# Optimization experiments

Measured on AMD Instinct MI355X. Metric: run time of the kernel, lower is better.

Reference implementation:

```python
import jax, jax.numpy as jnp
import numpy as np

N = 8192
IN_DIM = 512
MEM_DIM = 512


def _linear_params(k, fan_in, fan_out):
    kw, kb = jax.random.split(k)
    s = 1.0 / np.sqrt(fan_in)
    W = jax.random.uniform(kw, (fan_in, fan_out), jnp.float32, -s, s)
    b = jax.random.uniform(kb, (fan_out,), jnp.float32, -s, s)
    return W, b


def setup_inputs() -> dict:
    key = jax.random.key(0)
    ks = jax.random.split(key, 12)
    inputs = jax.random.normal(ks[0], (N, IN_DIM), jnp.float32)
    # tree.type is a [1,2] mixing matrix per node (lang vs vis weights)
    type_mask = jax.nn.softmax(jax.random.normal(ks[1], (N, 2), jnp.float32), axis=-1)
    # topologically ordered tree: parent slot of node i is in [0, i]; slot 0 = virtual zero root state
    rng = np.random.default_rng(0)
    parent = np.zeros(N, dtype=np.int32)
    for i in range(1, N):
        parent[i] = rng.integers(0, i + 1)
    d = {"inputs": inputs, "type_mask": type_mask, "parent": jnp.asarray(parent)}
    names = ["ioux_vis", "iouh_vis", "fx_vis", "fh_vis",
             "ioux_lang", "iouh_lang", "fx_lang", "fh_lang"]
    fanins = [IN_DIM, MEM_DIM, IN_DIM, MEM_DIM] * 2
    fanouts = [3 * MEM_DIM, 3 * MEM_DIM, MEM_DIM, MEM_DIM] * 2
    for j, nm in enumerate(names):
        W, b = _linear_params(ks[2 + j], fanins[j], fanouts[j])
        d["W_" + nm] = W
        d["b_" + nm] = b
    return d


def reference(inputs, type_mask, parent,
              W_ioux_vis, b_ioux_vis, W_iouh_vis, b_iouh_vis,
              W_fx_vis, b_fx_vis, W_fh_vis, b_fh_vis,
              W_ioux_lang, b_ioux_lang, W_iouh_lang, b_iouh_lang,
              W_fx_lang, b_fx_lang, W_fh_lang, b_fh_lang):
    n_nodes = inputs.shape[0]
    D = W_fh_vis.shape[1]
    # batch the input-dependent projections into big GEMMs (fused across all nodes)
    x_iou_v = inputs @ W_ioux_vis + b_ioux_vis  # [N, 3D]
    x_f_v = inputs @ W_fx_vis + b_fx_vis        # [N, D]
    x_iou_l = inputs @ W_ioux_lang + b_ioux_lang
    x_f_l = inputs @ W_fx_lang + b_fx_lang

    def node(x_iou, x_f, h_p, c_p, W_iouh, b_iouh, W_fh, b_fh):
        iou = x_iou + h_p @ W_iouh + b_iouh  # [3D]
        i, o, u = jnp.split(iou, 3)
        f = jax.nn.sigmoid(x_f + h_p @ W_fh + b_fh)
        c = jax.nn.sigmoid(i) * jnp.tanh(u) + f * c_p
        h = jax.nn.sigmoid(o) * jnp.tanh(c)
        return c, h

    # slot 0 holds the zero state used by root nodes; node i lives at slot i+1
    c0 = jnp.zeros((n_nodes + 1, D), inputs.dtype)
    h0 = jnp.zeros((n_nodes + 1, D), inputs.dtype)

    def step(carry, xs):
        c_all, h_all = carry
        n, p, xiv, xfv, xil, xfl, tm = xs
        h_p = h_all[p]
        c_p = c_all[p]
        c_v, h_v = node(xiv, xfv, h_p, c_p, W_iouh_vis, b_iouh_vis, W_fh_vis, b_fh_vis)
        c_l, h_l = node(xil, xfl, h_p, c_p, W_iouh_lang, b_iouh_lang, W_fh_lang, b_fh_lang)
        # type_mask @ cat([lang, vis]) == tm[0]*lang + tm[1]*vis
        c_n = tm[0] * c_l + tm[1] * c_v
        h_n = tm[0] * h_l + tm[1] * h_v  # dropout is identity in eval
        return (c_all.at[n + 1].set(c_n), h_all.at[n + 1].set(h_n)), None

    idx = jnp.arange(n_nodes)
    (c_all, h_all), _ = jax.lax.scan(
        step, (c0, h0), (idx, parent, x_iou_v, x_f_v, x_iou_l, x_f_l, type_mask))
    return c_all[1:], h_all[1:]
```

## Files before the change

### kernel.cpp

```cpp
#include <hip/hip_runtime.h>
#include <math.h>

typedef unsigned short ushort_t;
typedef unsigned int uint_t;
typedef unsigned long long u64_t;
typedef __attribute__((ext_vector_type(8))) short short8;
typedef __attribute__((ext_vector_type(4))) float f32x4;

#define N_NODES 8192
#define DIM 512
#define KTOT 1024
#define NCOLS 4096
#define BM 128
#define BN 128
#define NTILE (NCOLS / BN)
#define KIT (KTOT / 32)
#define WIMG_USHORTS ((size_t)NTILE * KIT * 4096)
#define MAXLEV_LDS 128
#define CSTRIDE 32

__device__ __forceinline__ float sigm(float x) { return 1.0f / (1.0f + __expf(-x)); }
__device__ __forceinline__ float tanh_fast(float x) {
    float ax = fabsf(x);
    float e = __expf(2.0f * ax);
    float t = 1.0f - 2.0f / (e + 1.0f);
    return copysignf(t, x);
}
__device__ __forceinline__ uint_t packf(float f) {
    uint_t u = __float_as_uint(f);
    uint_t hi = u & 0xffff0000u;
    float r = f - __uint_as_float(hi);
    return hi | (__float_as_uint(r) >> 16);
}
__device__ __forceinline__ float unpackw(uint_t w) {
    return __uint_as_float(w & 0xffff0000u) + __uint_as_float(w << 16);
}
__device__ __forceinline__ uint_t rne16(float f) {
    uint_t u = __float_as_uint(f);
    return (u + 0x7fffu + ((u >> 16) & 1u)) >> 16;
}

__device__ __forceinline__ void fragAB_u32(const uint4 w0, const uint4 w1,
                                           short8& hi8, short8& lo8) {
    union { uint_t w[4]; short8 s; } H, L;
    uint_t u[8] = { w0.x, w0.y, w0.z, w0.w, w1.x, w1.y, w1.z, w1.w };
#pragma unroll
    for (int j = 0; j < 4; ++j) {
        H.w[j] = (u[2 * j + 1] & 0xffff0000u) | (u[2 * j] >> 16);
        L.w[j] = (u[2 * j + 1] << 16) | (u[2 * j] & 0xffffu);
    }
    hi8 = H.s; lo8 = L.s;
}

__device__ __forceinline__ void fragA_f32(const float4 f0, const float4 f1,
                                          short8& hi8, short8& lo8) {
    union { uint_t w[4]; short8 s; } H, L;
    float f[8] = { f0.x, f0.y, f0.z, f0.w, f1.x, f1.y, f1.z, f1.w };
#pragma unroll
    for (int j = 0; j < 4; ++j) {
        float a = f[2 * j], b = f[2 * j + 1];
        uint_t h0 = __float_as_uint(a) & 0xffff0000u;
        uint_t h1 = __float_as_uint(b) & 0xffff0000u;
        float r0 = a - __uint_as_float(h0);
        float r1 = b - __uint_as_float(h1);
        H.w[j] = h1 | (h0 >> 16);
        L.w[j] = (__float_as_uint(r1) & 0xffff0000u) | (__float_as_uint(r0) >> 16);
    }
    hi8 = H.s; lo8 = L.s;
}

__global__ void __launch_bounds__(256) prep_wimg_kernel(
    const float* __restrict__ Wx_iou_v, const float* __restrict__ Wh_iou_v,
    const float* __restrict__ Wx_f_v,   const float* __restrict__ Wh_f_v,
    const float* __restrict__ Wx_iou_l, const float* __restrict__ Wh_iou_l,
    const float* __restrict__ Wx_f_l,   const float* __restrict__ Wh_f_l,
    ushort_t* __restrict__ Wimg)
{
    __shared__ float T[32][132];
    int p = blockIdx.x >> 5, it = blockIdx.x & 31;
    int tid = threadIdx.x;
#pragma unroll
    for (int e = 0; e < 16; ++e) {
        int lin = e * 256 + tid;
        int dloc = lin & 15, kk = (lin >> 4) & 31, q = lin >> 9;
        int d = p * 16 + dloc;
        int qq = q & 3; bool lang = q >= 4;
        int k = it * 32 + kk;
        const float* W; int col, stride;
        if (qq < 3) { col = qq * DIM + d; stride = 3 * DIM;
            W = (k < DIM) ? (lang ? Wx_iou_l : Wx_iou_v) : (lang ? Wh_iou_l : Wh_iou_v); }
        else        { col = d; stride = DIM;
            W = (k < DIM) ? (lang ? Wx_f_l : Wx_f_v) : (lang ? Wh_f_l : Wh_f_v); }
        int kr = (k < DIM) ? k : (k - DIM);
        T[kk][dloc * 8 + q] = W[(size_t)kr * stride + col];
    }
    __syncthreads();
    size_t tilebase = (size_t)blockIdx.x * 4096;
#pragma unroll
    for (int gch = 0; gch < 2; ++gch) {
        int gi = gch * 256 + tid;
        int col = gi >> 2, gd = gi & 3;
        uint_t wds[4];
#pragma unroll
        for (int i = 0; i < 4; ++i) {
            uint_t v0 = rne16(T[gd * 8 + 2 * i][col]);
            uint_t v1 = rne16(T[gd * 8 + 2 * i + 1][col]);
            wds[i] = (v1 << 16) | v0;
        }
        *(uint4*)(Wimg + tilebase + (size_t)gi * 8) = make_uint4(wds[0], wds[1], wds[2], wds[3]);
    }
}

__global__ void prep_bias_kernel(
    const float* __restrict__ bx_iou_v, const float* __restrict__ bh_iou_v,
    const float* __restrict__ bx_f_v,   const float* __restrict__ bh_f_v,
    const float* __restrict__ bx_iou_l, const float* __restrict__ bh_iou_l,
    const float* __restrict__ bx_f_l,   const float* __restrict__ bh_f_l,
    float* __restrict__ bias)
{
    int j = blockIdx.x * blockDim.x + threadIdx.x;
    if (j >= NCOLS) return;
    int d = j >> 3, q = j & 7;
    int qq = q & 3;
    bool lang = (q & 4) != 0;
    const float* bx; const float* bh; int col;
    if (qq < 3) { col = qq * DIM + d; bx = lang ? bx_iou_l : bx_iou_v; bh = lang ? bh_iou_l : bh_iou_v; }
    else        { col = d;            bx = lang ? bx_f_l  : bx_f_v;   bh = lang ? bh_f_l  : bh_f_v; }
    bias[j] = bx[col] + bh[col];
}

__global__ void __launch_bounds__(1024) levels_sort_kernel(
    const int* __restrict__ parent,
    int* __restrict__ order, int* __restrict__ offsets,
    int* __restrict__ counts, int* __restrict__ cursors,
    int* __restrict__ nlev, int* __restrict__ tilestart,
    int* __restrict__ rbStart)
{
    __shared__ int s_level[N_NODES];
    __shared__ int s_assigned;
    __shared__ int s_maxlev;
    int tid = threadIdx.x;
    int pr[8];
#pragma unroll
    for (int ii = 0; ii < 8; ++ii) {
        int i = tid + ii * 1024;
        pr[ii] = parent[i];
        s_level[i] = -1;
    }
    for (int i = tid; i <= N_NODES; i += 1024) counts[i] = 0;
    if (tid == 0) { s_assigned = 0; s_maxlev = 0; }
    __syncthreads();

    for (int pass = 0; pass <= N_NODES; ++pass) {
        int newly = 0;
#pragma unroll
        for (int ii = 0; ii < 8; ++ii) {
            int i = tid + ii * 1024;
            if (s_level[i] < 0) {
                int p = pr[ii];
                if (p == 0) { s_level[i] = 0; newly++; }
                else { int lp = s_level[p - 1]; if (lp >= 0) { s_level[i] = lp + 1; newly++; } }
            }
        }
        if (newly) atomicAdd(&s_assigned, newly);
        __syncthreads();
        int a = s_assigned;
        if (a >= N_NODES) break;
        __syncthreads();
    }

#pragma unroll
    for (int ii = 0; ii < 8; ++ii) {
        int i = tid + ii * 1024;
        int lv = s_level[i];
        atomicAdd(&counts[lv], 1);
        atomicMax(&s_maxlev, lv);
    }
    __syncthreads();
    if (tid == 0) {
        int nl = s_maxlev + 1;
        nlev[0] = nl;
        int off = 0, toff = 0, rb = 0;
        for (int l = 0; l < nl; ++l) {
            offsets[l] = off; cursors[l] = off;
            tilestart[l] = toff; rbStart[l] = rb;
            int mt = (counts[l] + BM - 1) / BM;
            rb += mt;
            toff += mt * NTILE;
            off += counts[l];
        }
        offsets[nl] = off;
        tilestart[nl] = toff;
        rbStart[nl] = rb;
        nlev[1] = toff;
    }
    __syncthreads();
#pragma unroll
    for (int ii = 0; ii < 8; ++ii) {
        int i = tid + ii * 1024;
        int pos = atomicAdd(&cursors[s_level[i]], 1);
        order[pos] = i;
    }
}

__global__ void __launch_bounds__(512, 2) tree_fused_kernel(
    const float* __restrict__ inputs, const float* __restrict__ type_mask,
    const ushort_t* __restrict__ Wimg, const float* __restrict__ bias,
    const int* __restrict__ order, const int* __restrict__ offsets,
    const int* __restrict__ nlev, const int* __restrict__ parent,
    const int* __restrict__ rbStart,
    int* __restrict__ colCnt,
    uint_t* __restrict__ hPack, uint_t* __restrict__ cPack,
    float* __restrict__ out)
{
    float* cOut = out;
    float* hOut = out + (size_t)N_NODES * DIM;

    __shared__ float eps[BM * 132];
    __shared__ int s_node[BM];
    __shared__ int s_par[BM];
    __shared__ float s_tm[BM][2];
    __shared__ int s_rbs[MAXLEV_LDS];
    __shared__ int s_off[MAXLEV_LDS];

    int tid = threadIdx.x;
    int lane = tid & 63, w = tid >> 6;
    int wr = w >> 1, wc = w & 1;
    int l15 = lane & 15, g = lane >> 4;
    int nl = nlev[0];
    int total = nlev[1];

    int nload = nl + 1; if (nload > MAXLEV_LDS) nload = MAXLEV_LDS;
    for (int i = tid; i < nload; i += 512) { s_rbs[i] = rbStart[i]; s_off[i] = offsets[i]; }
    __syncthreads();

    const ushort_t* bLane = Wimg + (size_t)(wc * 64 + l15) * 32 + (size_t)g * 8;

#define LDB(RB, tilebase, itt) { \
    _Pragma("unroll") for (int n_ = 0; n_ < 4; ++n_) \
        RB[n_] = *(const uint4*)(bLane + (size_t)(tilebase + (itt)) * 4096 + n_ * 512); }

#define LDA_H(RA, itrel) { \
    _Pragma("unroll") for (int m_ = 0; m_ < 2; ++m_) { \
        const uint4* p_ = (const uint4*)(aBaseH[m_] + (itrel) * 32 + g * 8); \
        RA[m_][0] = p_[0]; RA[m_][1] = p_[1]; } }

#define LDA_X(RA, itt) { \
    _Pragma("unroll") for (int m_ = 0; m_ < 2; ++m_) { \
        const float4* p_ = (const float4*)(aBaseX[m_] + (itt) * 32 + g * 8); \
        RA[m_][0] = p_[0]; RA[m_][1] = p_[1]; } }

#define COMP_H(RA, RB) { \
    short8 bh_[4]; \
    _Pragma("unroll") for (int n_ = 0; n_ < 4; ++n_) { \
        union { uint4 u; short8 s; } c_; c_.u = RB[n_]; bh_[n_] = c_.s; } \
    _Pragma("unroll") for (int m_ = 0; m_ < 2; ++m_) { \
        short8 ah_, al_; fragAB_u32(RA[m_][0], RA[m_][1], ah_, al_); \
        _Pragma("unroll") for (int n_ = 0; n_ < 4; ++n_) { \
            acc[m_][n_] = __builtin_amdgcn_mfma_f32_16x16x32_bf16(ah_, bh_[n_], acc[m_][n_], 0, 0, 0); \
            acc[m_][n_] = __builtin_amdgcn_mfma_f32_16x16x32_bf16(al_, bh_[n_], acc[m_][n_], 0, 0, 0); } } }

#define COMP_X(RA, RB) { \
    short8 bh_[4]; \
    _Pragma("unroll") for (int n_ = 0; n_ < 4; ++n_) { \
        union { uint4 u; short8 s; } c_; c_.u = RB[n_]; bh_[n_] = c_.s; } \
    _Pragma("unroll") for (int m_ = 0; m_ < 2; ++m_) { \
        short8 ah_, al_; fragA_f32(RA[m_][0], RA[m_][1], ah_, al_); \
        _Pragma("unroll") for (int n_ = 0; n_ < 4; ++n_) { \
            acc[m_][n_] = __builtin_amdgcn_mfma_f32_16x16x32_bf16(ah_, bh_[n_], acc[m_][n_], 0, 0, 0); \
            acc[m_][n_] = __builtin_amdgcn_mfma_f32_16x16x32_bf16(al_, bh_[n_], acc[m_][n_], 0, 0, 0); } } }

#define POLL_ALL(colPrev, nPrev) { \
    int ok_ = 1; \
    if (lane < 32) { \
        int c_ = __hip_atomic_load(&(colPrev)[lane * CSTRIDE], __ATOMIC_RELAXED, \
                                   __HIP_MEMORY_SCOPE_AGENT); \
        ok_ = (c_ >= (nPrev)) ? 1 : 0; \
    } \
    uint_t cm_ = (uint_t)(__ballot(ok_) & 0xffffffffu); \
    uint_t gr_ = cm_ & (cm_ >> 1) & (cm_ >> 2) & (cm_ >> 3); \
    gmask = 0; \
    _Pragma("unroll") for (int g_ = 0; g_ < 8; ++g_) \
        gmask |= ((gr_ >> (4 * g_)) & 1u) << g_; }

#define WAVE_GATE(colPrev, nPrev, gq, slp) { \
    if (!(gmask & (1u << (gq)))) { \
        for (;;) { \
            POLL_ALL(colPrev, nPrev); \
            if (gmask & (1u << (gq))) break; \
            __builtin_amdgcn_s_sleep(slp); \
        } \
        asm volatile("" ::: "memory"); \
    } }

    for (int t = blockIdx.x; t < total; t += gridDim.x) {
        int lev = 0;
        while (lev + 1 < nload && s_rbs[lev + 1] * NTILE <= t) ++lev;
        int lt = t - s_rbs[lev] * NTILE;
        int ntile = lt % NTILE;
        int mt = lt / NTILE;
        int start = s_off[lev];
        int cnt = s_off[lev + 1] - start;
        int jc = ntile * BN;
        int r0 = mt * BM;
        int tbx = ntile * KIT;
        int tbh = ntile * KIT + 16;

        if (tid < BM) {
            int r = r0 + tid;
            int node = (r < cnt) ? order[start + r] : -1;
            s_node[tid] = node;
            int p = (node >= 0) ? parent[node] : 0;
            s_par[tid] = p;
            float t0 = 0.f, t1 = 0.f;
            if (node >= 0) { t0 = type_mask[node * 2]; t1 = type_mask[node * 2 + 1]; }
            s_tm[tid][0] = t0; s_tm[tid][1] = t1;
        }
        __syncthreads();

        f32x4 acc[2][4];
#pragma unroll
        for (int m = 0; m < 2; ++m)
#pragma unroll
            for (int n = 0; n < 4; ++n) acc[m][n] = (f32x4)(0.f);

        {
            const float* aBaseX[2];
#pragma unroll
            for (int m = 0; m < 2; ++m) {
                int nd = s_node[wr * 32 + m * 16 + l15];
                aBaseX[m] = inputs + (size_t)(nd < 0 ? 0 : nd) * DIM;
            }
            float4 xa0[2][2], xa1[2][2]; uint4 xb0[4], xb1[4];
            LDA_X(xa0, 0); LDB(xb0, tbx, 0);
            LDA_X(xa1, 1); LDB(xb1, tbx, 1);
#pragma unroll
            for (int ii = 0; ii < 8; ++ii) {
                int e = 2 * ii, o = e + 1;
                __builtin_amdgcn_s_setprio(1);
                COMP_X(xa0, xb0);
                __builtin_amdgcn_s_setprio(0);
                if (e + 2 < 16) { LDA_X(xa0, e + 2); LDB(xb0, tbx, e + 2); }
                __builtin_amdgcn_s_setprio(1);
                COMP_X(xa1, xb1);
                __builtin_amdgcn_s_setprio(0);
                if (o + 2 < 16) { LDA_X(xa1, o + 2); LDB(xb1, tbx, o + 2); }
            }
        }

        if (lev > 0) {
            const int* colPrev = colCnt + (size_t)(lev - 1) * NTILE * CSTRIDE;
            int nPrev = s_rbs[lev] - s_rbs[lev - 1];
            const int gb = ntile >> 2;
            uint_t gmask = 0;

            const uint_t* aBaseH[2];
#pragma unroll
            for (int m = 0; m < 2; ++m) {
                int p = s_par[wr * 32 + m * 16 + l15];
                aBaseH[m] = hPack + (size_t)((p > 0) ? (p - 1) : 0) * DIM;
            }

            uint4 ha0[2][2], ha1[2][2]; uint4 hb0[4], hb1[4];
            WAVE_GATE(colPrev, nPrev, gb, 4);
            LDA_H(ha0, 2 * gb); LDB(hb0, tbh, 2 * gb);
            LDA_H(ha1, 2 * gb + 1); LDB(hb1, tbh, 2 * gb + 1);
#pragma unroll
            for (int s = 0; s < 8; ++s) {
                const int gn = (gb + s + 1) & 7;
                __builtin_amdgcn_s_setprio(1);
                COMP_H(ha0, hb0);
                __builtin_amdgcn_s_setprio(0);
                if (s < 7) {
                    WAVE_GATE(colPrev, nPrev, gn, 2);
                    LDA_H(ha0, 2 * gn); LDB(hb0, tbh, 2 * gn);
                }
                __builtin_amdgcn_s_setprio(1);
                COMP_H(ha1, hb1);
                __builtin_amdgcn_s_setprio(0);
                if (s < 7) { LDA_H(ha1, 2 * gn + 1); LDB(hb1, tbh, 2 * gn + 1); }
            }
        }

        int cntloc = cnt - r0; if (cntloc > BM) cntloc = BM;
        int erow = tid >> 2, qd = tid & 3;
        int dbase = (jc >> 3) + qd * 4;

        float CPv[4];
        {
            int p = (erow < cntloc) ? s_par[erow] : 0;
            uint4 cw = make_uint4(0u, 0u, 0u, 0u);
            if (p > 0) cw = *(const uint4*)(cPack + (size_t)(p - 1) * DIM + dbase);
            CPv[0] = unpackw(cw.x); CPv[1] = unpackw(cw.y);
            CPv[2] = unpackw(cw.z); CPv[3] = unpackw(cw.w);
        }

#pragma unroll
        for (int m = 0; m < 2; ++m)
#pragma unroll
            for (int n = 0; n < 4; ++n) {
                int row = wr * 32 + m * 16 + g * 4;
                int c = wc * 64 + n * 16 + l15;
#pragma unroll
                for (int r = 0; r < 4; ++r) eps[(row + r) * 132 + c] = acc[m][n][r];
            }
        __syncthreads();

        float cn4[4], hn4[4];
        int enode = -1;
        if (erow < cntloc) {
            enode = s_node[erow];
            const float* ep = &eps[erow * 132 + qd * 32];
            float tm0 = s_tm[erow][0], tm1 = s_tm[erow][1];
            float cpl[4] = { CPv[0], CPv[1], CPv[2], CPv[3] };
#pragma unroll
            for (int j = 0; j < 4; ++j) {
                float4 v0 = *(const float4*)(ep + j * 8);
                float4 v1 = *(const float4*)(ep + j * 8 + 4);
                int jb = jc + (qd * 4 + j) * 8;
                float4 b0 = *(const float4*)(bias + jb);
                float4 b1 = *(const float4*)(bias + jb + 4);
                float cp = cpl[j];
                float cv = sigm(v0.x + b0.x) * tanh_fast(v0.z + b0.z)
                         + sigm(v0.w + b0.w) * cp;
                float hv = sigm(v0.y + b0.y) * tanh_fast(cv);
                float cl = sigm(v1.x + b1.x) * tanh_fast(v1.z + b1.z)
                         + sigm(v1.w + b1.w) * cp;
                float hl = sigm(v1.y + b1.y) * tanh_fast(cl);
                cn4[j] = tm0 * cl + tm1 * cv;
                hn4[j] = tm0 * hl + tm1 * hv;
            }
            size_t oi = (size_t)enode * DIM + dbase;
            u64_t c01 = (u64_t)packf(cn4[0]) | ((u64_t)packf(cn4[1]) << 32);
            u64_t c23 = (u64_t)packf(cn4[2]) | ((u64_t)packf(cn4[3]) << 32);
            u64_t h01 = (u64_t)packf(hn4[0]) | ((u64_t)packf(hn4[1]) << 32);
            u64_t h23 = (u64_t)packf(hn4[2]) | ((u64_t)packf(hn4[3]) << 32);
            u64_t* cdst = (u64_t*)(cPack + oi);
            u64_t* hdst = (u64_t*)(hPack + oi);
            __hip_atomic_store(cdst,     c01, __ATOMIC_RELAXED, __HIP_MEMORY_SCOPE_AGENT);
            __hip_atomic_store(cdst + 1, c23, __ATOMIC_RELAXED, __HIP_MEMORY_SCOPE_AGENT);
            __hip_atomic_store(hdst,     h01, __ATOMIC_RELAXED, __HIP_MEMORY_SCOPE_AGENT);
            __hip_atomic_store(hdst + 1, h23, __ATOMIC_RELAXED, __HIP_MEMORY_SCOPE_AGENT);
        }

        __builtin_amdgcn_s_waitcnt(0);
        __syncthreads();
        if (tid == 0)
            __hip_atomic_fetch_add(&colCnt[(size_t)(lev * NTILE + ntile) * CSTRIDE], 1,
                                   __ATOMIC_RELAXED, __HIP_MEMORY_SCOPE_AGENT);

        if (enode >= 0) {
            size_t oi = (size_t)enode * DIM + dbase;
            *(float4*)(cOut + oi) = make_float4(cn4[0], cn4[1], cn4[2], cn4[3]);
            *(float4*)(hOut + oi) = make_float4(hn4[0], hn4[1], hn4[2], hn4[3]);
        }
        __syncthreads();
    }
#undef LDB
#undef LDA_H
#undef LDA_X
#undef COMP_H
#undef COMP_X
#undef POLL_ALL
#undef WAVE_GATE
}

extern "C" void kernel_launch(void* const* d_in, const int* in_sizes, int n_in,
                              void* d_out, int out_size, void* d_ws, size_t ws_size,
                              hipStream_t stream) {
    const float* inputs      = (const float*)d_in[0];
    const float* type_mask   = (const float*)d_in[1];
    const int*   parent      = (const int*)d_in[2];
    const float* W_ioux_vis  = (const float*)d_in[3];
    const float* b_ioux_vis  = (const float*)d_in[4];
    const float* W_iouh_vis  = (const float*)d_in[5];
    const float* b_iouh_vis  = (const float*)d_in[6];
    const float* W_fx_vis    = (const float*)d_in[7];
    const float* b_fx_vis    = (const float*)d_in[8];
    const float* W_fh_vis    = (const float*)d_in[9];
    const float* b_fh_vis    = (const float*)d_in[10];
    const float* W_ioux_lang = (const float*)d_in[11];
    const float* b_ioux_lang = (const float*)d_in[12];
    const float* W_iouh_lang = (const float*)d_in[13];
    const float* b_iouh_lang = (const float*)d_in[14];
    const float* W_fx_lang   = (const float*)d_in[15];
    const float* b_fx_lang   = (const float*)d_in[16];
    const float* W_fh_lang   = (const float*)d_in[17];
    const float* b_fh_lang   = (const float*)d_in[18];

    ushort_t* Wimg = (ushort_t*)d_ws;
    float* bias    = (float*)(Wimg + WIMG_USHORTS);
    int* order     = (int*)(bias + NCOLS);
    int* offsets   = order + N_NODES;
    int* counts    = offsets + (N_NODES + 2);
    int* cursors   = counts + (N_NODES + 2);
    int* nlev      = cursors + (N_NODES + 2);
    int* tilestart = nlev + 8;
    int* rbStart   = tilestart + (N_NODES + 2);
    size_t cOff = (size_t)((char*)(rbStart + (N_NODES + 2)) - (char*)d_ws);
    cOff = (cOff + 127) & ~(size_t)127;
    int* colCnt = (int*)((char*)d_ws + cOff);
    size_t off2 = cOff + (size_t)MAXLEV_LDS * NTILE * CSTRIDE * sizeof(int);
    off2 = (off2 + 255) & ~(size_t)255;
    uint_t* hPack = (uint_t*)((char*)d_ws + off2);
    uint_t* cPack = hPack + (size_t)N_NODES * DIM;

    float* out = (float*)d_out;

    hipMemsetAsync((void*)colCnt, 0, (size_t)MAXLEV_LDS * NTILE * CSTRIDE * sizeof(int), stream);

    hipLaunchKernelGGL(prep_wimg_kernel, dim3(NTILE * KIT), dim3(256), 0, stream,
                       W_ioux_vis, W_iouh_vis, W_fx_vis, W_fh_vis,
                       W_ioux_lang, W_iouh_lang, W_fx_lang, W_fh_lang, Wimg);
    hipLaunchKernelGGL(prep_bias_kernel, dim3(NCOLS / 256), dim3(256), 0, stream,
                       b_ioux_vis, b_iouh_vis, b_fx_vis, b_fh_vis,
                       b_ioux_lang, b_iouh_lang, b_fx_lang, b_fh_lang, bias);
    hipLaunchKernelGGL(levels_sort_kernel, dim3(1), dim3(1024), 0, stream,
                       parent, order, offsets, counts, cursors, nlev, tilestart,
                       rbStart);

    int occ = 0;
    if (hipOccupancyMaxActiveBlocksPerMultiprocessor(&occ, (const void*)tree_fused_kernel, 512, 0) != hipSuccess || occ < 1)
        occ = 1;
    int bpc = occ < 2 ? occ : 2;
    dim3 grid(256 * bpc);

    void* args[] = { (void*)&inputs, (void*)&type_mask, (void*)&Wimg, (void*)&bias,
                     (void*)&order, (void*)&offsets, (void*)&nlev, (void*)&parent,
                     (void*)&rbStart, (void*)&colCnt,
                     (void*)&hPack, (void*)&cPack, (void*)&out };
    hipLaunchCooperativeKernel((const void*)tree_fused_kernel, grid, dim3(512), args, 0, stream);
}
```

Measured before the change: 743.3 us.

## Split input projection into a producer queue overlapped with level-ordered recurrent tiles

The input-projection GEMM is split out of each per-level tile and run as a separate work queue. Three quarters of the blocks compute all X tiles up front and store them packed to a workspace buffer with per-tile ready flags. All blocks then pull recurrent H tiles from an atomic counter, wait on the matching X flags, and add the stored projection in the epilogue. This takes the input GEMM off the dependency-chained critical path. The parent c state is now read from the fp32 output instead of a packed copy, and the cost is extra global traffic for the X-activation buffer plus flag polling.

```diff
diff --git a/kernel.cpp b/kernel.cpp
--- a/kernel.cpp
+++ b/kernel.cpp
@@ -15,6 +15,8 @@
 #define BN 128
 #define NTILE (NCOLS / BN)
 #define KIT (KTOT / 32)
+#define XRB (N_NODES / BM)
+#define XTILES (XRB * NTILE)
 #define WIMG_USHORTS ((size_t)NTILE * KIT * 4096)
 #define MAXLEV_LDS 128
 #define CSTRIDE 32
@@ -203,14 +205,13 @@
     }
 }
 
-__global__ void __launch_bounds__(512, 2) tree_fused_kernel(
+__global__ void __launch_bounds__(512, 2) tree_xq_kernel(
     const float* __restrict__ inputs, const float* __restrict__ type_mask,
     const ushort_t* __restrict__ Wimg, const float* __restrict__ bias,
     const int* __restrict__ order, const int* __restrict__ offsets,
     const int* __restrict__ nlev, const int* __restrict__ parent,
-    const int* __restrict__ rbStart,
-    int* __restrict__ colCnt,
-    uint_t* __restrict__ hPack, uint_t* __restrict__ cPack,
+    const int* __restrict__ rbStart, int* __restrict__ ctr,
+    uint_t* __restrict__ hPack, uint_t* __restrict__ xAct,
     float* __restrict__ out)
 {
     float* cOut = out;
@@ -222,13 +223,19 @@
     __shared__ float s_tm[BM][2];
     __shared__ int s_rbs[MAXLEV_LDS];
     __shared__ int s_off[MAXLEV_LDS];
+    __shared__ int s_t;
 
     int tid = threadIdx.x;
     int lane = tid & 63, w = tid >> 6;
     int wr = w >> 1, wc = w & 1;
     int l15 = lane & 15, g = lane >> 4;
     int nl = nlev[0];
-    int total = nlev[1];
+    int totalH = nlev[1];
+
+    int* xCur   = ctr;
+    int* hCur   = ctr + CSTRIDE;
+    int* xFlag  = ctr + 2 * CSTRIDE;
+    int* colCnt = xFlag + (size_t)XTILES * CSTRIDE;
 
     int nload = nl + 1; if (nload > MAXLEV_LDS) nload = MAXLEV_LDS;
     for (int i = tid; i < nload; i += 512) { s_rbs[i] = rbStart[i]; s_off[i] = offsets[i]; }
@@ -293,44 +300,31 @@
         asm volatile("" ::: "memory"); \
     } }
 
-    for (int t = blockIdx.x; t < total; t += gridDim.x) {
-        int lev = 0;
-        while (lev + 1 < nload && s_rbs[lev + 1] * NTILE <= t) ++lev;
-        int lt = t - s_rbs[lev] * NTILE;
-        int ntile = lt % NTILE;
-        int mt = lt / NTILE;
-        int start = s_off[lev];
-        int cnt = s_off[lev + 1] - start;
-        int jc = ntile * BN;
-        int r0 = mt * BM;
-        int tbx = ntile * KIT;
-        int tbh = ntile * KIT + 16;
-
-        if (tid < BM) {
-            int r = r0 + tid;
-            int node = (r < cnt) ? order[start + r] : -1;
-            s_node[tid] = node;
-            int p = (node >= 0) ? parent[node] : 0;
-            s_par[tid] = p;
-            float t0 = 0.f, t1 = 0.f;
-            if (node >= 0) { t0 = type_mask[node * 2]; t1 = type_mask[node * 2 + 1]; }
-            s_tm[tid][0] = t0; s_tm[tid][1] = t1;
-        }
-        __syncthreads();
-
-        f32x4 acc[2][4];
-#pragma unroll
-        for (int m = 0; m < 2; ++m)
-#pragma unroll
-            for (int n = 0; n < 4; ++n) acc[m][n] = (f32x4)(0.f);
-
-        {
+    if (blockIdx.x < (gridDim.x * 3) / 4) {
+        for (;;) {
+            if (tid == 0)
+                s_t = __hip_atomic_fetch_add(xCur, 1, __ATOMIC_RELAXED, __HIP_MEMORY_SCOPE_AGENT);
+            __syncthreads();
+            int t = s_t;
+            if (t >= XTILES) break;
+            int ntile = t & (NTILE - 1), rb = t >> 5;
+            int jc = ntile * BN, pos0 = rb * BM;
+            int tbx = ntile * KIT;
+
+            if (tid < BM) s_node[tid] = order[pos0 + tid];
+            __syncthreads();
+
+            f32x4 acc[2][4];
+#pragma unroll
+            for (int m = 0; m < 2; ++m)
+#pragma unroll
+                for (int n = 0; n < 4; ++n) acc[m][n] = (f32x4)(0.f);
+
             const float* aBaseX[2];
 #pragma unroll
-            for (int m = 0; m < 2; ++m) {
-                int nd = s_node[wr * 32 + m * 16 + l15];
-                aBaseX[m] = inputs + (size_t)(nd < 0 ? 0 : nd) * DIM;
-            }
+            for (int m = 0; m < 2; ++m)
+                aBaseX[m] = inputs + (size_t)s_node[wr * 32 + m * 16 + l15] * DIM;
+
             float4 xa0[2][2], xa1[2][2]; uint4 xb0[4], xb1[4];
             LDA_X(xa0, 0); LDB(xb0, tbx, 0);
             LDA_X(xa1, 1); LDB(xb1, tbx, 1);
@@ -346,7 +340,73 @@
                 __builtin_amdgcn_s_setprio(0);
                 if (o + 2 < 16) { LDA_X(xa1, o + 2); LDB(xb1, tbx, o + 2); }
             }
-        }
+
+            __syncthreads();
+#pragma unroll
+            for (int m = 0; m < 2; ++m)
+#pragma unroll
+                for (int n = 0; n < 4; ++n) {
+                    int row = wr * 32 + m * 16 + g * 4;
+                    int c = wc * 64 + n * 16 + l15;
+#pragma unroll
+                    for (int r = 0; r < 4; ++r) eps[(row + r) * 132 + c] = acc[m][n][r];
+                }
+            __syncthreads();
+            {
+                int erow = tid >> 2, qd = tid & 3;
+                const float* ep = &eps[erow * 132 + qd * 32];
+                u64_t* dst = (u64_t*)(xAct + (size_t)(pos0 + erow) * NCOLS + jc + qd * 32);
+#pragma unroll
+                for (int j = 0; j < 16; ++j) {
+                    u64_t v = (u64_t)packf(ep[2 * j]) | ((u64_t)packf(ep[2 * j + 1]) << 32);
+                    __hip_atomic_store(dst + j, v, __ATOMIC_RELAXED, __HIP_MEMORY_SCOPE_AGENT);
+                }
+            }
+            __builtin_amdgcn_s_waitcnt(0);
+            __syncthreads();
+            if (tid == 0)
+                __hip_atomic_store(&xFlag[(size_t)t * CSTRIDE], 1,
+                                   __ATOMIC_RELAXED, __HIP_MEMORY_SCOPE_AGENT);
+            __syncthreads();
+        }
+    }
+
+    for (;;) {
+        if (tid == 0)
+            s_t = __hip_atomic_fetch_add(hCur, 1, __ATOMIC_RELAXED, __HIP_MEMORY_SCOPE_AGENT);
+        __syncthreads();
+        int t = s_t;
+        if (t >= totalH) break;
+
+        int lev = 0;
+        while (lev + 1 < nload && s_rbs[lev + 1] * NTILE <= t) ++lev;
+        int lt = t - s_rbs[lev] * NTILE;
+        int ntile = lt % NTILE;
+        int mt = lt / NTILE;
+        int start = s_off[lev];
+        int cnt = s_off[lev + 1] - start;
+        int jc = ntile * BN;
+        int r0 = mt * BM;
+        int tbh = ntile * KIT + 16;
+        int cntloc = cnt - r0; if (cntloc > BM) cntloc = BM;
+
+        if (tid < BM) {
+            int r = r0 + tid;
+            int node = (r < cnt) ? order[start + r] : -1;
+            s_node[tid] = node;
+            int p = (node >= 0) ? parent[node] : 0;
+            s_par[tid] = p;
+            float t0 = 0.f, t1 = 0.f;
+            if (node >= 0) { t0 = type_mask[node * 2]; t1 = type_mask[node * 2 + 1]; }
+            s_tm[tid][0] = t0; s_tm[tid][1] = t1;
+        }
+        __syncthreads();
+
+        f32x4 acc[2][4];
+#pragma unroll
+        for (int m = 0; m < 2; ++m)
+#pragma unroll
+            for (int n = 0; n < 4; ++n) acc[m][n] = (f32x4)(0.f);
 
         if (lev > 0) {
             const int* colPrev = colCnt + (size_t)(lev - 1) * NTILE * CSTRIDE;
@@ -382,17 +442,42 @@
             }
         }
 
-        int cntloc = cnt - r0; if (cntloc > BM) cntloc = BM;
+        {
+            int prb0 = (start + r0) >> 7;
+            int prb1 = (start + r0 + ((cntloc > 0) ? (cntloc - 1) : 0)) >> 7;
+            if (tid == 0) {
+                while (__hip_atomic_load(&xFlag[(size_t)(prb0 * NTILE + ntile) * CSTRIDE],
+                                         __ATOMIC_RELAXED, __HIP_MEMORY_SCOPE_AGENT) == 0)
+                    __builtin_amdgcn_s_sleep(1);
+            }
+            if (tid == 1 && prb1 != prb0) {
+                while (__hip_atomic_load(&xFlag[(size_t)(prb1 * NTILE + ntile) * CSTRIDE],
+                                         __ATOMIC_RELAXED, __HIP_MEMORY_SCOPE_AGENT) == 0)
+                    __builtin_amdgcn_s_sleep(1);
+            }
+            __syncthreads();
+            asm volatile("" ::: "memory");
+        }
+
         int erow = tid >> 2, qd = tid & 3;
         int dbase = (jc >> 3) + qd * 4;
 
         float CPv[4];
         {
             int p = (erow < cntloc) ? s_par[erow] : 0;
-            uint4 cw = make_uint4(0u, 0u, 0u, 0u);
-            if (p > 0) cw = *(const uint4*)(cPack + (size_t)(p - 1) * DIM + dbase);
-            CPv[0] = unpackw(cw.x); CPv[1] = unpackw(cw.y);
-            CPv[2] = unpackw(cw.z); CPv[3] = unpackw(cw.w);
+            float4 cw = make_float4(0.f, 0.f, 0.f, 0.f);
+            if (p > 0) cw = *(const float4*)(cOut + (size_t)(p - 1) * DIM + dbase);
+            CPv[0] = cw.x; CPv[1] = cw.y; CPv[2] = cw.z; CPv[3] = cw.w;
+        }
+        float xv[32];
+        if (erow < cntloc) {
+            const uint4* xs = (const uint4*)(xAct + (size_t)(start + r0 + erow) * NCOLS + jc + qd * 32);
+#pragma unroll
+            for (int q = 0; q < 8; ++q) {
+                uint4 wv = xs[q];
+                xv[q * 4 + 0] = unpackw(wv.x); xv[q * 4 + 1] = unpackw(wv.y);
+                xv[q * 4 + 2] = unpackw(wv.z); xv[q * 4 + 3] = unpackw(wv.w);
+            }
         }
 
 #pragma unroll
@@ -412,15 +497,18 @@
             enode = s_node[erow];
             const float* ep = &eps[erow * 132 + qd * 32];
             float tm0 = s_tm[erow][0], tm1 = s_tm[erow][1];
-            float cpl[4] = { CPv[0], CPv[1], CPv[2], CPv[3] };
 #pragma unroll
             for (int j = 0; j < 4; ++j) {
                 float4 v0 = *(const float4*)(ep + j * 8);
                 float4 v1 = *(const float4*)(ep + j * 8 + 4);
+                v0.x += xv[j * 8 + 0]; v0.y += xv[j * 8 + 1];
+                v0.z += xv[j * 8 + 2]; v0.w += xv[j * 8 + 3];
+                v1.x += xv[j * 8 + 4]; v1.y += xv[j * 8 + 5];
+                v1.z += xv[j * 8 + 6]; v1.w += xv[j * 8 + 7];
                 int jb = jc + (qd * 4 + j) * 8;
                 float4 b0 = *(const float4*)(bias + jb);
                 float4 b1 = *(const float4*)(bias + jb + 4);
-                float cp = cpl[j];
+                float cp = CPv[j];
                 float cv = sigm(v0.x + b0.x) * tanh_fast(v0.z + b0.z)
                          + sigm(v0.w + b0.w) * cp;
                 float hv = sigm(v0.y + b0.y) * tanh_fast(cv);
@@ -431,11 +519,11 @@
                 hn4[j] = tm0 * hl + tm1 * hv;
             }
             size_t oi = (size_t)enode * DIM + dbase;
-            u64_t c01 = (u64_t)packf(cn4[0]) | ((u64_t)packf(cn4[1]) << 32);
-            u64_t c23 = (u64_t)packf(cn4[2]) | ((u64_t)packf(cn4[3]) << 32);
+            u64_t c01 = (u64_t)__float_as_uint(cn4[0]) | ((u64_t)__float_as_uint(cn4[1]) << 32);
+            u64_t c23 = (u64_t)__float_as_uint(cn4[2]) | ((u64_t)__float_as_uint(cn4[3]) << 32);
             u64_t h01 = (u64_t)packf(hn4[0]) | ((u64_t)packf(hn4[1]) << 32);
             u64_t h23 = (u64_t)packf(hn4[2]) | ((u64_t)packf(hn4[3]) << 32);
-            u64_t* cdst = (u64_t*)(cPack + oi);
+            u64_t* cdst = (u64_t*)(cOut + oi);
             u64_t* hdst = (u64_t*)(hPack + oi);
             __hip_atomic_store(cdst,     c01, __ATOMIC_RELAXED, __HIP_MEMORY_SCOPE_AGENT);
             __hip_atomic_store(cdst + 1, c23, __ATOMIC_RELAXED, __HIP_MEMORY_SCOPE_AGENT);
@@ -451,7 +539,6 @@
 
         if (enode >= 0) {
             size_t oi = (size_t)enode * DIM + dbase;
-            *(float4*)(cOut + oi) = make_float4(cn4[0], cn4[1], cn4[2], cn4[3]);
             *(float4*)(hOut + oi) = make_float4(hn4[0], hn4[1], hn4[2], hn4[3]);
         }
         __syncthreads();
@@ -499,15 +586,16 @@
     int* rbStart   = tilestart + (N_NODES + 2);
     size_t cOff = (size_t)((char*)(rbStart + (N_NODES + 2)) - (char*)d_ws);
     cOff = (cOff + 127) & ~(size_t)127;
-    int* colCnt = (int*)((char*)d_ws + cOff);
-    size_t off2 = cOff + (size_t)MAXLEV_LDS * NTILE * CSTRIDE * sizeof(int);
+    int* ctr = (int*)((char*)d_ws + cOff);
+    const size_t CTRI = (size_t)(2 + XTILES + MAXLEV_LDS * NTILE) * CSTRIDE;
+    size_t off2 = cOff + CTRI * sizeof(int);
     off2 = (off2 + 255) & ~(size_t)255;
     uint_t* hPack = (uint_t*)((char*)d_ws + off2);
-    uint_t* cPack = hPack + (size_t)N_NODES * DIM;
+    uint_t* xAct  = hPack + (size_t)N_NODES * DIM;
 
     float* out = (float*)d_out;
 
-    hipMemsetAsync((void*)colCnt, 0, (size_t)MAXLEV_LDS * NTILE * CSTRIDE * sizeof(int), stream);
+    hipMemsetAsync((void*)ctr, 0, CTRI * sizeof(int), stream);
 
     hipLaunchKernelGGL(prep_wimg_kernel, dim3(NTILE * KIT), dim3(256), 0, stream,
                        W_ioux_vis, W_iouh_vis, W_fx_vis, W_fh_vis,
@@ -520,14 +608,14 @@
                        rbStart);
 
     int occ = 0;
-    if (hipOccupancyMaxActiveBlocksPerMultiprocessor(&occ, (const void*)tree_fused_kernel, 512, 0) != hipSuccess || occ < 1)
+    if (hipOccupancyMaxActiveBlocksPerMultiprocessor(&occ, (const void*)tree_xq_kernel, 512, 0) != hipSuccess || occ < 1)
         occ = 1;
     int bpc = occ < 2 ? occ : 2;
     dim3 grid(256 * bpc);
 
     void* args[] = { (void*)&inputs, (void*)&type_mask, (void*)&Wimg, (void*)&bias,
                      (void*)&order, (void*)&offsets, (void*)&nlev, (void*)&parent,
-                     (void*)&rbStart, (void*)&colCnt,
-                     (void*)&hPack, (void*)&cPack, (void*)&out };
-    hipLaunchCooperativeKernel((const void*)tree_fused_kernel, grid, dim3(512), args, 0, stream);
-}
+                     (void*)&rbStart, (void*)&ctr,
+                     (void*)&hPack, (void*)&xAct, (void*)&out };
+    hipLaunchCooperativeKernel((const void*)tree_xq_kernel, grid, dim3(512), args, 0, stream);
+}
```

Measured after the change: 897.5 us. +20.7%, slower.
